# Performance work log

Measured on AMD Instinct MI355X. Metric: run time of the kernel, lower is better.

The kernel has to match this reference:

```python
import jax, jax.numpy as jnp
import numpy as np

ALPHA = 0.2  # LeakyReLU negative slope
B, N, F, T, H, D = 4, 2048, 256, 8, 4, 64


def setup_inputs() -> dict:
    key = jax.random.key(0)
    ks = jax.random.split(key, 8)
    x = jax.random.normal(ks[0], (B, N, F), dtype=jnp.float32)
    adj = jax.random.randint(ks[1], (B, N, N), 0, 2, dtype=jnp.int32)
    type_idx = jax.random.randint(ks[2], (B, N), 0, T)
    type_onehot = jax.nn.one_hot(type_idx, T, dtype=jnp.float32)
    # per-head parameters stacked on a leading head axis (original uses H separate layers)
    s = 0.06  # ~xavier_uniform scale for these fan sizes
    Wq = jax.random.normal(ks[3], (H, F + T, D), dtype=jnp.float32) * s
    Wk = jax.random.normal(ks[4], (H, F + T, D), dtype=jnp.float32) * s
    W = jax.random.normal(ks[5], (H, F, D), dtype=jnp.float32) * s
    a = jax.random.normal(ks[6], (H, 2 * D, 1), dtype=jnp.float32) * s
    return {"x": x, "adj": adj, "type_onehot": type_onehot,
            "Wq": Wq, "Wk": Wk, "W": W, "a": a}


def reference(x, adj, type_onehot, Wq, Wk, W, a):
    # eval mode: dropout is identity
    nh, d = W.shape[0], W.shape[2]
    h_t = jnp.concatenate([x, type_onehot], axis=-1)           # (B,N,F+T)
    q = jnp.einsum('bnf,hfd->bhnd', h_t, Wq)                   # (B,H,N,D)
    k = jnp.einsum('bnf,hfd->bhnd', h_t, Wk)                   # (B,H,N,D)
    a1 = a[:, :d, 0]                                           # (H,D)
    a2 = a[:, d:, 0]                                           # (H,D)
    e1 = jnp.einsum('bhnd,hd->bhn', q, a1)                     # (B,H,N)
    e2 = jnp.einsum('bhnd,hd->bhn', k, a2)                     # (B,H,N)
    e = e1[:, :, :, None] + e2[:, :, None, :]                  # (B,H,N,N) additive score
    e = jnp.where(e > 0, e, ALPHA * e)                         # leaky relu
    mask = (adj > 0)[:, None, :, :]                            # (B,1,N,N)
    att = jnp.where(mask, e, jnp.float32(-9e15))
    att = jax.nn.softmax(att, axis=2)                          # torch dim=1 of (B,N,N) == axis 2 here
    att = att * adj[:, None, :, :].astype(att.dtype)
    Wh = jnp.einsum('bnf,hfd->bhnd', x, W)                     # (B,H,N,D)
    h_prime = jnp.einsum('bhij,bhjd->bhid', att, Wh)           # (B,H,N,D)
    out = jax.nn.elu(h_prime)                                  # concat=True per head
    # concat heads on feature dim, matching torch.cat([...], dim=2)
    return out.transpose(0, 2, 1, 3).reshape(x.shape[0], x.shape[1], nh * d)
```

## Files before the change

### kernel.cpp

```cpp
#include <hip/hip_runtime.h>
#include <hip/hip_bf16.h>
#include <math.h>

#define ALPHA 0.2f
#define LOG2E 1.4426950408889634f

constexpr int B_ = 4, N_ = 2048, F_ = 256, T_ = 8, H_ = 4, D_ = 64;
constexpr int FT = F_ + T_;

using half8   = __attribute__((ext_vector_type(8))) _Float16;
using half2v  = __attribute__((ext_vector_type(2))) _Float16;
using float4v = __attribute__((ext_vector_type(4))) float;
using uint4v  = __attribute__((ext_vector_type(4))) unsigned;

#if __has_builtin(__builtin_amdgcn_exp2f)
#define EXP2F(x) __builtin_amdgcn_exp2f(x)
#else
#define EXP2F(x) exp2f(x)
#endif

__device__ inline unsigned pkrtz_u(float a, float b) {
    return __builtin_bit_cast(unsigned, __builtin_amdgcn_cvt_pkrtz(a, b));
}

#define V1_OFF    0u
#define V2_OFF    4224u
#define E1A_OFF   8448u
#define E2A_OFF   270592u
#define PC_OFF    532736u
#define NC_OFF    663808u
#define PARTS_OFF 794880u
#define WT_OFF    2892032u
#define BITS_OFF  3023104u
#define WHT_OFF   5120256u

__device__ inline void gl2lds16(const void* g, void* l) {
    __builtin_amdgcn_global_load_lds(
        (const __attribute__((address_space(1))) unsigned*)g,
        (__attribute__((address_space(3))) unsigned*)l, 16, 0, 0);
}

__global__ __launch_bounds__(256) void k_adjpack(const int* __restrict__ adj,
                                                 unsigned* __restrict__ bits) {
    size_t tid = (size_t)blockIdx.x * 256 + threadIdx.x;
    int av = adj[tid];
    unsigned long long msk = __ballot(av != 0);
    int lane = threadIdx.x & 63;
    if (lane == 0)       bits[tid >> 5] = (unsigned)msk;
    else if (lane == 32) bits[tid >> 5] = (unsigned)(msk >> 32);
}

__global__ __launch_bounds__(256) void k_prep(const float* __restrict__ Wq,
                                              const float* __restrict__ Wk,
                                              const float* __restrict__ a,
                                              const float* __restrict__ W,
                                              float* __restrict__ v1,
                                              float* __restrict__ v2,
                                              _Float16* __restrict__ WT) {
    int gid = blockIdx.x * 256 + threadIdx.x;
    if (gid < 65536) {
        int hd = gid >> 8, f = gid & 255;
        int h = hd >> 6, d = hd & 63;
        WT[(size_t)hd * F_ + f] = (_Float16)W[((size_t)h * F_ + f) * D_ + d];
        return;
    }
    int tid = gid - 65536;
    if (tid >= 2 * H_ * FT) return;
    int sel = tid / (H_ * FT);
    int r = tid - sel * (H_ * FT);
    int h = r / FT, f = r - h * FT;
    const float* Wx = sel ? Wk : Wq;
    const float* av = a + h * 2 * D_ + sel * D_;
    const float* wrow = Wx + (size_t)(h * FT + f) * D_;
    float acc = 0.f;
    for (int d = 0; d < D_; ++d) acc += wrow[d] * av[d];
    (sel ? v2 : v1)[h * FT + f] = acc * LOG2E;
}

__global__ __launch_bounds__(256) void k_e12(const float* __restrict__ x,
                                             const float* __restrict__ oh,
                                             const float* __restrict__ v1,
                                             const float* __restrict__ v2,
                                             float2* __restrict__ E1A,
                                             float2* __restrict__ E2A) {
    int lane = threadIdx.x & 63;
    int w = threadIdx.x >> 6;
    int bn = blockIdx.x * 4 + w;
    int b = bn >> 11, n = bn & (N_ - 1);
    float a1h[H_] = {0.f, 0.f, 0.f, 0.f};
    float a2h[H_] = {0.f, 0.f, 0.f, 0.f};
    const float* xrow = x + (size_t)(b * N_ + n) * F_;
    for (int c = 0; c < 4; ++c) {
        int f = c * 64 + lane;
        float xv = xrow[f];
        #pragma unroll
        for (int h = 0; h < H_; ++h) {
            a1h[h] += xv * v1[h * FT + f];
            a2h[h] += xv * v2[h * FT + f];
        }
    }
    if (lane < T_) {
        float ov = oh[(size_t)(b * N_ + n) * T_ + lane];
        #pragma unroll
        for (int h = 0; h < H_; ++h) {
            a1h[h] += ov * v1[h * FT + F_ + lane];
            a2h[h] += ov * v2[h * FT + F_ + lane];
        }
    }
    #pragma unroll
    for (int off = 32; off; off >>= 1) {
        #pragma unroll
        for (int h = 0; h < H_; ++h) {
            a1h[h] += __shfl_xor(a1h[h], off, 64);
            a2h[h] += __shfl_xor(a2h[h], off, 64);
        }
    }
    if (lane == 0) {
        #pragma unroll
        for (int h = 0; h < H_; ++h) {
            size_t o = (size_t)(b * H_ + h) * N_ + n;
            E1A[o] = {EXP2F(a1h[h]), EXP2F(ALPHA * a1h[h])};
            E2A[o] = {EXP2F(a2h[h]), EXP2F(ALPHA * a2h[h])};
        }
    }
}

__global__ __launch_bounds__(256) void k_wht(const float* __restrict__ x,
                                             const _Float16* __restrict__ WT,
                                             _Float16* __restrict__ WhT) {
    int lane = threadIdx.x;
    int h = threadIdx.y;
    int jt = blockIdx.x;
    int b  = blockIdx.y;
    int j0 = jt * 16;
    int m = lane & 15, quad = lane >> 4;
    float4v zero = {0.f, 0.f, 0.f, 0.f};
    float4v acc[4] = {zero, zero, zero, zero};
    #pragma unroll 2
    for (int f0 = 0; f0 < F_; f0 += 32) {
        const float* xp = x + (size_t)(b * N_ + j0 + m) * F_ + f0 + quad * 8;
        float4v xlo = *(const float4v*)xp;
        float4v xhi = *(const float4v*)(xp + 4);
        uint4v bp = {pkrtz_u(xlo[0], xlo[1]), pkrtz_u(xlo[2], xlo[3]),
                     pkrtz_u(xhi[0], xhi[1]), pkrtz_u(xhi[2], xhi[3])};
        half8 bfrag = __builtin_bit_cast(half8, bp);
        #pragma unroll
        for (int mt = 0; mt < 4; ++mt) {
            const _Float16* ap = WT + (size_t)(h * 64 + mt * 16 + m) * F_ + f0 + quad * 8;
            half8 afrag = *(const half8*)ap;
            acc[mt] = __builtin_amdgcn_mfma_f32_16x16x32_f16(afrag, bfrag, acc[mt], 0, 0, 0);
        }
    }
    #pragma unroll
    for (int mt = 0; mt < 4; ++mt) {
        #pragma unroll
        for (int reg = 0; reg < 4; ++reg) {
            int hd = h * 64 + mt * 16 + quad * 4 + reg;
            WhT[((size_t)b * 256 + hd) * N_ + j0 + m] = (_Float16)acc[mt][reg];
        }
    }
}

__global__ __launch_bounds__(256) void k_colsum(const unsigned* __restrict__ bits,
                                                const float2* __restrict__ E1A,
                                                const float2* __restrict__ E2A,
                                                float* __restrict__ part_s) {
    int tid = threadIdx.x;
    int jt = blockIdx.x, b = blockIdx.y, ic = blockIdx.z;
    int j = jt * 256 + tid;
    int i0 = ic * 128;
    float2 e2v[H_];
    float acc[H_] = {0.f, 0.f, 0.f, 0.f};
    #pragma unroll
    for (int h = 0; h < H_; ++h) e2v[h] = E2A[(size_t)(b * H_ + h) * N_ + j];
    const float2* e1b = E1A + (size_t)(b * H_) * N_;
    const unsigned* bp = bits + ((size_t)(b * N_ + i0)) * 64 + (j >> 5);
    unsigned sh = j & 31;
    #pragma unroll 8
    for (int k = 0; k < 128; ++k) {
        unsigned wv = bp[(size_t)k * 64];
        bool on = (wv >> sh) & 1u;
        int i = i0 + k;
        #pragma unroll
        for (int h = 0; h < H_; ++h) {
            float2 e1 = e1b[h * N_ + i];
            float t = fmaxf(e1.x * e2v[h].x, e1.y * e2v[h].y);
            acc[h] += on ? t : 0.f;
        }
    }
    #pragma unroll
    for (int h = 0; h < H_; ++h)
        part_s[(size_t)ic * (B_ * H_ * N_) + (size_t)(b * H_ + h) * N_ + j] = acc[h];
}

__global__ __launch_bounds__(256) void k_scale(const float* __restrict__ part_s,
                                               const float2* __restrict__ E2A,
                                               float* __restrict__ pc,
                                               float* __restrict__ nc) {
    int tid = blockIdx.x * 256 + threadIdx.x;
    float s = 0.f;
    #pragma unroll
    for (int ic = 0; ic < 16; ++ic) s += part_s[(size_t)ic * (B_ * H_ * N_) + tid];
    float c = (s > 0.f) ? 1.f / s : 0.f;
    float2 e2 = E2A[tid];
    pc[tid] = e2.x * c;
    nc[tid] = e2.y * c;
}

__global__ __launch_bounds__(256, 2) void k_main(const unsigned* __restrict__ bits,
                                                 const float2* __restrict__ E1A,
                                                 const float* __restrict__ pc_g,
                                                 const float* __restrict__ nc_g,
                                                 const _Float16* __restrict__ WhT,
                                                 float* __restrict__ out) {
    __shared__ float sPC[2048];
    __shared__ float sNC[2048];
    __shared__ unsigned sLUT[256][4];
    __shared__ _Float16 sW[2][8192];
    int lane = threadIdx.x;
    int wy = threadIdx.y;
    int it = blockIdx.x;
    int b  = blockIdx.y;
    int h  = blockIdx.z;
    int ibase = it * 64 + wy * 16;
    int m = lane & 15, quad = lane >> 4;
    int bh = b * H_ + h;
    int t256 = wy * 64 + lane;

    {
        unsigned t = t256;
        sLUT[t][0] = ((t & 1u) ? 0xFFFFu : 0u) | ((t & 2u) ? 0xFFFF0000u : 0u);
        sLUT[t][1] = ((t & 4u) ? 0xFFFFu : 0u) | ((t & 8u) ? 0xFFFF0000u : 0u);
        sLUT[t][2] = ((t & 16u) ? 0xFFFFu : 0u) | ((t & 32u) ? 0xFFFF0000u : 0u);
        sLUT[t][3] = ((t & 64u) ? 0xFFFFu : 0u) | ((t & 128u) ? 0xFFFF0000u : 0u);
        int base = t256 * 8;
        *(float4v*)&sPC[base]     = *(const float4v*)(pc_g + (size_t)bh * N_ + base);
        *(float4v*)&sPC[base + 4] = *(const float4v*)(pc_g + (size_t)bh * N_ + base + 4);
        *(float4v*)&sNC[base]     = *(const float4v*)(nc_g + (size_t)bh * N_ + base);
        *(float4v*)&sNC[base + 4] = *(const float4v*)(nc_g + (size_t)bh * N_ + base + 4);
    }
    float2 e1v = E1A[(size_t)bh * N_ + ibase + m];
    const _Float16* bbase = WhT + (size_t)(b * 256 + h * 64) * N_;
    const unsigned* brow = bits + ((size_t)(b * N_) + ibase + m) * 64;

    auto stage = [&](int buf, int jb) {
        #pragma unroll
        for (int q = 0; q < 4; ++q) {
            int r = q * 16 + wy * 4 + (lane >> 4);
            int g = (lane & 15) ^ (r & 15);
            const _Float16* gp = bbase + (size_t)r * N_ + jb + g * 8;
            void* lp = (void*)&sW[buf][q * 2048 + wy * 512];
            gl2lds16(gp, lp);
        }
    };

    stage(0, 0);
    __syncthreads();

    float4v zero = {0.f, 0.f, 0.f, 0.f};
    float4v acc[4] = {zero, zero, zero, zero};

    for (int k = 0; k < 16; ++k) {
        if (k < 15) stage((k + 1) & 1, (k + 1) * 128);
        uint4v bwv = *(const uint4v*)(brow + k * 4);
        #pragma unroll
        for (int u = 0; u < 4; ++u) {
            unsigned byte = (bwv[u] >> (quad * 8)) & 0xFFu;
            uint4v msk = *(const uint4v*)&sLUT[byte][0];
            int jg = k * 128 + u * 32 + quad * 8;
            float4v p0 = *(const float4v*)&sPC[jg];
            float4v p1 = *(const float4v*)&sPC[jg + 4];
            float4v n0 = *(const float4v*)&sNC[jg];
            float4v n1 = *(const float4v*)&sNC[jg + 4];
            float w[8];
            #pragma unroll
            for (int e = 0; e < 4; ++e) w[e]     = fmaxf(e1v.x * p0[e], e1v.y * n0[e]);
            #pragma unroll
            for (int e = 0; e < 4; ++e) w[4 + e] = fmaxf(e1v.x * p1[e], e1v.y * n1[e]);
            uint4v wvp = {pkrtz_u(w[0], w[1]) & msk[0], pkrtz_u(w[2], w[3]) & msk[1],
                          pkrtz_u(w[4], w[5]) & msk[2], pkrtz_u(w[6], w[7]) & msk[3]};
            half8 afrag = __builtin_bit_cast(half8, wvp);
            #pragma unroll
            for (int dt = 0; dt < 4; ++dt) {
                int r = dt * 16 + m;
                int segp = (u * 4 + quad) ^ m;
                half8 bfrag = *(const half8*)&sW[k & 1][r * 128 + segp * 8];
                acc[dt] = __builtin_amdgcn_mfma_f32_16x16x32_f16(afrag, bfrag, acc[dt], 0, 0, 0);
            }
        }
        __syncthreads();
    }

    #pragma unroll
    for (int dt = 0; dt < 4; ++dt) {
        #pragma unroll
        for (int reg = 0; reg < 4; ++reg) {
            int i = ibase + quad * 4 + reg;
            int d = dt * 16 + m;
            float v = acc[dt][reg];
            v = v > 0.f ? v : expm1f(v);
            out[((size_t)(b * N_ + i)) * (H_ * D_) + h * D_ + d] = v;
        }
    }
}

extern "C" void kernel_launch(void* const* d_in, const int* in_sizes, int n_in,
                              void* d_out, int out_size, void* d_ws, size_t ws_size,
                              hipStream_t stream) {
    const float* x   = (const float*)d_in[0];
    const int*   adj = (const int*)d_in[1];
    const float* oh  = (const float*)d_in[2];
    const float* Wq  = (const float*)d_in[3];
    const float* Wk  = (const float*)d_in[4];
    const float* W   = (const float*)d_in[5];
    const float* a   = (const float*)d_in[6];
    float* out = (float*)d_out;
    char* ws = (char*)d_ws;

    float*   v1    = (float*)(ws + V1_OFF);
    float*   v2    = (float*)(ws + V2_OFF);
    float2*  E1A   = (float2*)(ws + E1A_OFF);
    float2*  E2A   = (float2*)(ws + E2A_OFF);
    float*   pc    = (float*)(ws + PC_OFF);
    float*   nc    = (float*)(ws + NC_OFF);
    float*   parts = (float*)(ws + PARTS_OFF);
    _Float16* WT   = (_Float16*)(ws + WT_OFF);
    unsigned* bits = (unsigned*)(ws + BITS_OFF);
    _Float16* WhT  = (_Float16*)(ws + WHT_OFF);

    k_adjpack<<<65536, 256, 0, stream>>>(adj, bits);
    k_prep<<<265, 256, 0, stream>>>(Wq, Wk, a, W, v1, v2, WT);
    k_e12<<<B_ * N_ / 4, 256, 0, stream>>>(x, oh, v1, v2, E1A, E2A);
    k_wht<<<dim3(128, 4), dim3(64, 4), 0, stream>>>(x, WT, WhT);
    k_colsum<<<dim3(8, 4, 16), 256, 0, stream>>>(bits, E1A, E2A, parts);
    k_scale<<<128, 256, 0, stream>>>(parts, E2A, pc, nc);
    k_main<<<dim3(32, 4, 4), dim3(64, 4), 0, stream>>>(bits, E1A, pc, nc, WhT, out);
}
```

Before: 185.5 us.

## Merge independent launches and fold partial-sum scaling into main kernel

Combines adjacency bit-packing with weight prep into one launch, and the e1/e2 score computation with the Wh projection into another, using block-index ranges to pick the role. The separate scale kernel is dropped: each k_main block now reduces the 16 column-sum partials and computes the normalisation coefficients into shared memory. This cuts the launch count from seven to four and removes the pc/nc round trip through global memory. In exchange, every k_main block redundantly re-reads the partials for its (b,h), and the heterogeneous blocks in the merged launches may be scheduled less evenly.

```diff
diff --git a/kernel.cpp b/kernel.cpp
--- a/kernel.cpp
+++ b/kernel.cpp
@@ -9,7 +9,6 @@
 constexpr int FT = F_ + T_;
 
 using half8   = __attribute__((ext_vector_type(8))) _Float16;
-using half2v  = __attribute__((ext_vector_type(2))) _Float16;
 using float4v = __attribute__((ext_vector_type(4))) float;
 using uint4v  = __attribute__((ext_vector_type(4))) unsigned;
 
@@ -27,8 +26,6 @@
 #define V2_OFF    4224u
 #define E1A_OFF   8448u
 #define E2A_OFF   270592u
-#define PC_OFF    532736u
-#define NC_OFF    663808u
 #define PARTS_OFF 794880u
 #define WT_OFF    2892032u
 #define BITS_OFF  3023104u
@@ -40,24 +37,25 @@
         (__attribute__((address_space(3))) unsigned*)l, 16, 0, 0);
 }
 
-__global__ __launch_bounds__(256) void k_adjpack(const int* __restrict__ adj,
-                                                 unsigned* __restrict__ bits) {
-    size_t tid = (size_t)blockIdx.x * 256 + threadIdx.x;
-    int av = adj[tid];
-    unsigned long long msk = __ballot(av != 0);
-    int lane = threadIdx.x & 63;
-    if (lane == 0)       bits[tid >> 5] = (unsigned)msk;
-    else if (lane == 32) bits[tid >> 5] = (unsigned)(msk >> 32);
-}
-
-__global__ __launch_bounds__(256) void k_prep(const float* __restrict__ Wq,
-                                              const float* __restrict__ Wk,
-                                              const float* __restrict__ a,
-                                              const float* __restrict__ W,
-                                              float* __restrict__ v1,
-                                              float* __restrict__ v2,
-                                              _Float16* __restrict__ WT) {
-    int gid = blockIdx.x * 256 + threadIdx.x;
+__global__ __launch_bounds__(256) void k_pre(const int* __restrict__ adj,
+                                             const float* __restrict__ Wq,
+                                             const float* __restrict__ Wk,
+                                             const float* __restrict__ a,
+                                             const float* __restrict__ W,
+                                             unsigned* __restrict__ bits,
+                                             float* __restrict__ v1,
+                                             float* __restrict__ v2,
+                                             _Float16* __restrict__ WT) {
+    if (blockIdx.x < 65536u) {
+        size_t tid = (size_t)blockIdx.x * 256 + threadIdx.x;
+        int av = adj[tid];
+        unsigned long long msk = __ballot(av != 0);
+        int lane = threadIdx.x & 63;
+        if (lane == 0)       bits[tid >> 5] = (unsigned)msk;
+        else if (lane == 32) bits[tid >> 5] = (unsigned)(msk >> 32);
+        return;
+    }
+    int gid = (blockIdx.x - 65536) * 256 + threadIdx.x;
     if (gid < 65536) {
         int hd = gid >> 8, f = gid & 255;
         int h = hd >> 6, d = hd & 63;
@@ -77,61 +75,61 @@
     (sel ? v2 : v1)[h * FT + f] = acc * LOG2E;
 }
 
-__global__ __launch_bounds__(256) void k_e12(const float* __restrict__ x,
+__global__ __launch_bounds__(256) void k_mid(const float* __restrict__ x,
                                              const float* __restrict__ oh,
                                              const float* __restrict__ v1,
                                              const float* __restrict__ v2,
+                                             const _Float16* __restrict__ WT,
                                              float2* __restrict__ E1A,
-                                             float2* __restrict__ E2A) {
+                                             float2* __restrict__ E2A,
+                                             _Float16* __restrict__ WhT) {
+    if (blockIdx.x < 2048u) {
+        int lane = threadIdx.x & 63;
+        int w = threadIdx.x >> 6;
+        int bn = blockIdx.x * 4 + w;
+        int b = bn >> 11, n = bn & (N_ - 1);
+        float a1h[H_] = {0.f, 0.f, 0.f, 0.f};
+        float a2h[H_] = {0.f, 0.f, 0.f, 0.f};
+        const float* xrow = x + (size_t)(b * N_ + n) * F_;
+        for (int c = 0; c < 4; ++c) {
+            int f = c * 64 + lane;
+            float xv = xrow[f];
+            #pragma unroll
+            for (int h = 0; h < H_; ++h) {
+                a1h[h] += xv * v1[h * FT + f];
+                a2h[h] += xv * v2[h * FT + f];
+            }
+        }
+        if (lane < T_) {
+            float ov = oh[(size_t)(b * N_ + n) * T_ + lane];
+            #pragma unroll
+            for (int h = 0; h < H_; ++h) {
+                a1h[h] += ov * v1[h * FT + F_ + lane];
+                a2h[h] += ov * v2[h * FT + F_ + lane];
+            }
+        }
+        #pragma unroll
+        for (int off = 32; off; off >>= 1) {
+            #pragma unroll
+            for (int h = 0; h < H_; ++h) {
+                a1h[h] += __shfl_xor(a1h[h], off, 64);
+                a2h[h] += __shfl_xor(a2h[h], off, 64);
+            }
+        }
+        if (lane == 0) {
+            #pragma unroll
+            for (int h = 0; h < H_; ++h) {
+                size_t o = (size_t)(b * H_ + h) * N_ + n;
+                E1A[o] = {EXP2F(a1h[h]), EXP2F(ALPHA * a1h[h])};
+                E2A[o] = {EXP2F(a2h[h]), EXP2F(ALPHA * a2h[h])};
+            }
+        }
+        return;
+    }
+    int bid = blockIdx.x - 2048;
+    int jt = bid & 127, b = bid >> 7;
     int lane = threadIdx.x & 63;
-    int w = threadIdx.x >> 6;
-    int bn = blockIdx.x * 4 + w;
-    int b = bn >> 11, n = bn & (N_ - 1);
-    float a1h[H_] = {0.f, 0.f, 0.f, 0.f};
-    float a2h[H_] = {0.f, 0.f, 0.f, 0.f};
-    const float* xrow = x + (size_t)(b * N_ + n) * F_;
-    for (int c = 0; c < 4; ++c) {
-        int f = c * 64 + lane;
-        float xv = xrow[f];
-        #pragma unroll
-        for (int h = 0; h < H_; ++h) {
-            a1h[h] += xv * v1[h * FT + f];
-            a2h[h] += xv * v2[h * FT + f];
-        }
-    }
-    if (lane < T_) {
-        float ov = oh[(size_t)(b * N_ + n) * T_ + lane];
-        #pragma unroll
-        for (int h = 0; h < H_; ++h) {
-            a1h[h] += ov * v1[h * FT + F_ + lane];
-            a2h[h] += ov * v2[h * FT + F_ + lane];
-        }
-    }
-    #pragma unroll
-    for (int off = 32; off; off >>= 1) {
-        #pragma unroll
-        for (int h = 0; h < H_; ++h) {
-            a1h[h] += __shfl_xor(a1h[h], off, 64);
-            a2h[h] += __shfl_xor(a2h[h], off, 64);
-        }
-    }
-    if (lane == 0) {
-        #pragma unroll
-        for (int h = 0; h < H_; ++h) {
-            size_t o = (size_t)(b * H_ + h) * N_ + n;
-            E1A[o] = {EXP2F(a1h[h]), EXP2F(ALPHA * a1h[h])};
-            E2A[o] = {EXP2F(a2h[h]), EXP2F(ALPHA * a2h[h])};
-        }
-    }
-}
-
-__global__ __launch_bounds__(256) void k_wht(const float* __restrict__ x,
-                                             const _Float16* __restrict__ WT,
-                                             _Float16* __restrict__ WhT) {
-    int lane = threadIdx.x;
-    int h = threadIdx.y;
-    int jt = blockIdx.x;
-    int b  = blockIdx.y;
+    int h = threadIdx.x >> 6;
     int j0 = jt * 16;
     int m = lane & 15, quad = lane >> 4;
     float4v zero = {0.f, 0.f, 0.f, 0.f};
@@ -193,24 +191,10 @@
         part_s[(size_t)ic * (B_ * H_ * N_) + (size_t)(b * H_ + h) * N_ + j] = acc[h];
 }
 
-__global__ __launch_bounds__(256) void k_scale(const float* __restrict__ part_s,
-                                               const float2* __restrict__ E2A,
-                                               float* __restrict__ pc,
-                                               float* __restrict__ nc) {
-    int tid = blockIdx.x * 256 + threadIdx.x;
-    float s = 0.f;
-    #pragma unroll
-    for (int ic = 0; ic < 16; ++ic) s += part_s[(size_t)ic * (B_ * H_ * N_) + tid];
-    float c = (s > 0.f) ? 1.f / s : 0.f;
-    float2 e2 = E2A[tid];
-    pc[tid] = e2.x * c;
-    nc[tid] = e2.y * c;
-}
-
 __global__ __launch_bounds__(256, 2) void k_main(const unsigned* __restrict__ bits,
                                                  const float2* __restrict__ E1A,
-                                                 const float* __restrict__ pc_g,
-                                                 const float* __restrict__ nc_g,
+                                                 const float2* __restrict__ E2A,
+                                                 const float* __restrict__ parts,
                                                  const _Float16* __restrict__ WhT,
                                                  float* __restrict__ out) {
     __shared__ float sPC[2048];
@@ -234,10 +218,30 @@
         sLUT[t][2] = ((t & 16u) ? 0xFFFFu : 0u) | ((t & 32u) ? 0xFFFF0000u : 0u);
         sLUT[t][3] = ((t & 64u) ? 0xFFFFu : 0u) | ((t & 128u) ? 0xFFFF0000u : 0u);
         int base = t256 * 8;
-        *(float4v*)&sPC[base]     = *(const float4v*)(pc_g + (size_t)bh * N_ + base);
-        *(float4v*)&sPC[base + 4] = *(const float4v*)(pc_g + (size_t)bh * N_ + base + 4);
-        *(float4v*)&sNC[base]     = *(const float4v*)(nc_g + (size_t)bh * N_ + base);
-        *(float4v*)&sNC[base + 4] = *(const float4v*)(nc_g + (size_t)bh * N_ + base + 4);
+        float4v s0 = {0.f, 0.f, 0.f, 0.f}, s1 = {0.f, 0.f, 0.f, 0.f};
+        #pragma unroll
+        for (int ic = 0; ic < 16; ++ic) {
+            const float* pp = parts + (size_t)ic * (B_ * H_ * N_) + (size_t)bh * N_ + base;
+            s0 += *(const float4v*)pp;
+            s1 += *(const float4v*)(pp + 4);
+        }
+        const float2* e2p = E2A + (size_t)bh * N_ + base;
+        #pragma unroll
+        for (int e = 0; e < 4; ++e) {
+            float s = s0[e];
+            float c = (s > 0.f) ? 1.f / s : 0.f;
+            float2 e2 = e2p[e];
+            sPC[base + e] = e2.x * c;
+            sNC[base + e] = e2.y * c;
+        }
+        #pragma unroll
+        for (int e = 0; e < 4; ++e) {
+            float s = s1[e];
+            float c = (s > 0.f) ? 1.f / s : 0.f;
+            float2 e2 = e2p[4 + e];
+            sPC[base + 4 + e] = e2.x * c;
+            sNC[base + 4 + e] = e2.y * c;
+        }
     }
     float2 e1v = E1A[(size_t)bh * N_ + ibase + m];
     const _Float16* bbase = WhT + (size_t)(b * 256 + h * 64) * N_;
@@ -321,18 +325,13 @@
     float*   v2    = (float*)(ws + V2_OFF);
     float2*  E1A   = (float2*)(ws + E1A_OFF);
     float2*  E2A   = (float2*)(ws + E2A_OFF);
-    float*   pc    = (float*)(ws + PC_OFF);
-    float*   nc    = (float*)(ws + NC_OFF);
     float*   parts = (float*)(ws + PARTS_OFF);
     _Float16* WT   = (_Float16*)(ws + WT_OFF);
     unsigned* bits = (unsigned*)(ws + BITS_OFF);
     _Float16* WhT  = (_Float16*)(ws + WHT_OFF);
 
-    k_adjpack<<<65536, 256, 0, stream>>>(adj, bits);
-    k_prep<<<265, 256, 0, stream>>>(Wq, Wk, a, W, v1, v2, WT);
-    k_e12<<<B_ * N_ / 4, 256, 0, stream>>>(x, oh, v1, v2, E1A, E2A);
-    k_wht<<<dim3(128, 4), dim3(64, 4), 0, stream>>>(x, WT, WhT);
+    k_pre<<<65536 + 265, 256, 0, stream>>>(adj, Wq, Wk, a, W, bits, v1, v2, WT);
+    k_mid<<<2048 + 512, 256, 0, stream>>>(x, oh, v1, v2, WT, E1A, E2A, WhT);
     k_colsum<<<dim3(8, 4, 16), 256, 0, stream>>>(bits, E1A, E2A, parts);
-    k_scale<<<128, 256, 0, stream>>>(parts, E2A, pc, nc);
-    k_main<<<dim3(32, 4, 4), dim3(64, 4), 0, stream>>>(bits, E1A, pc, nc, WhT, out);
-}
+    k_main<<<dim3(32, 4, 4), dim3(64, 4), 0, stream>>>(bits, E1A, E2A, parts, WhT, out);
+}
```

New measurement: 187.4 us. Within noise of the previous version (+1.0%).
